# Kernel optimization log

Hardware: AMD Instinct MI355X
Metric: run time of the kernel (lower is better)

## Reference

```python
import jax, jax.numpy as jnp
import numpy as np

HIDDEN = 1024
NUM_HEADS = 16
D_HEAD = HIDDEN // NUM_HEADS  # 64
SEQ = 2048
BATCH = 2


def setup_inputs() -> dict:
    key = jax.random.key(0)
    kx, kw, kb = jax.random.split(key, 3)
    x = jax.random.normal(kx, (SEQ, BATCH, HIDDEN), dtype=jnp.float32)
    W = jax.random.normal(kw, (3 * HIDDEN, HIDDEN), dtype=jnp.float32) * 0.02
    b = jax.random.normal(kb, (3 * HIDDEN,), dtype=jnp.float32) * 0.02
    return {"x": x, "W": W, "b": b}


def reference(x, W, b):
    # x: (S, B, H) seq-first, as in the torch module
    S, B, _ = x.shape
    qkv = jnp.einsum('sbh,oh->sbo', x, W) + b  # (S, B, 3*H)
    # torch views 3*hidden as (num_heads, 3, d_head): per-head-interleaved QKV
    qkv = qkv.reshape(S, B, NUM_HEADS, 3, D_HEAD)
    qkv = jnp.transpose(qkv, (2, 1, 0, 3, 4))  # (nh, B, S, 3, d)
    q, k, v = qkv[..., 0, :], qkv[..., 1, :], qkv[..., 2, :]  # each (nh, B, S, d)
    scale = 1.0 / np.sqrt(D_HEAD).astype(np.float32)
    scores = jnp.einsum('hbqd,hbkd->hbqk', q, k) * scale  # (nh, B, S, S)
    attn = jax.nn.softmax(scores, axis=-1)
    out = jnp.einsum('hbqk,hbkd->hbqd', attn, v)  # (nh, B, S, d)
    out = jnp.transpose(out, (2, 1, 0, 3)).reshape(S, B, HIDDEN)
    return out
```

## Files before the change

### kernel.cpp

```cpp
#include <hip/hip_runtime.h>
#include <hip/hip_bf16.h>


typedef __hip_bfloat16 bf16;
typedef __bf16 bfr;
typedef __attribute__((ext_vector_type(8))) __bf16 bf16x8;
typedef __attribute__((ext_vector_type(4))) __bf16 bf16x4;
typedef __attribute__((ext_vector_type(4))) float f32x4;

#define S_SEQ  2048
#define HID    1024
#define OUT3   3072
#define NROWS  4096
#define LSTR   72

#if __has_builtin(__builtin_amdgcn_exp2f)
#define EXP2F(x) __builtin_amdgcn_exp2f(x)
#else
#define EXP2F(x) exp2f(x)
#endif

#define QSCALE 0.18033688011112042f

__global__ __launch_bounds__(256) void cast_both_kernel(
    const float* __restrict__ X, bfr* __restrict__ Xb,
    const float* __restrict__ W, bfr* __restrict__ Wb)
{
    int bid = blockIdx.x;
    const float* src;
    bfr* dst;
    int lid;
    if (bid < NROWS * HID / 2048) { src = X; dst = Xb; lid = bid; }
    else { src = W; dst = Wb; lid = bid - NROWS * HID / 2048; }
    int gid = lid * 256 + threadIdx.x;
    const float4* s4 = (const float4*)src;
    float4 a = s4[(size_t)gid * 2];
    float4 b = s4[(size_t)gid * 2 + 1];
    bf16x8 v;
    v[0] = (bfr)a.x; v[1] = (bfr)a.y; v[2] = (bfr)a.z; v[3] = (bfr)a.w;
    v[4] = (bfr)b.x; v[5] = (bfr)b.y; v[6] = (bfr)b.z; v[7] = (bfr)b.w;
    *(bf16x8*)(dst + (size_t)gid * 8) = v;
}

__device__ __forceinline__ void gload_lds16(const void* g, void* l) {
    __builtin_amdgcn_global_load_lds(
        (const __attribute__((address_space(1))) unsigned int*)g,
        (__attribute__((address_space(3))) unsigned int*)l, 16, 0, 0);
}

__global__ __launch_bounds__(256, 3) void qkv_gemm_mfma(
    const bfr* __restrict__ Xb, const bfr* __restrict__ Wb,
    const float* __restrict__ bias,
    bfr* __restrict__ qb, bfr* __restrict__ kb, bfr* __restrict__ vtb)
{
    __shared__ __attribute__((aligned(16))) unsigned char lds_all[32768];
    bfr* As = (bfr*)lds_all;
    bfr* Bs = (bfr*)(lds_all + 16384);
    bfr* Tr = (bfr*)lds_all;

    const int o0 = blockIdx.x * 128;
    const int r0 = blockIdx.y * 128;
    const int tid = threadIdx.x;
    const int lane = tid & 63;
    const int w = tid >> 6;
    const int l15 = lane & 15;
    const int quad = lane >> 4;
    const int m0 = (w & 1) * 64;
    const int n0 = (w >> 1) * 64;

    f32x4 acc[4][4];
#pragma unroll
    for (int mi = 0; mi < 4; mi++)
#pragma unroll
        for (int ni = 0; ni < 4; ni++) acc[mi][ni] = {0.f, 0.f, 0.f, 0.f};

    for (int k0 = 0; k0 < HID; k0 += 64) {
#pragma unroll
        for (int i = 0; i < 4; i++) {
            int c = i * 256 + tid;
            int row = c >> 3, c8 = c & 7;
            gload_lds16(Xb + (size_t)(r0 + row) * HID + k0 + c8 * 8, As + c * 8);
            gload_lds16(Wb + (size_t)(o0 + row) * HID + k0 + c8 * 8, Bs + c * 8);
        }
        __syncthreads();

#pragma unroll
        for (int ks = 0; ks < 2; ks++) {
            bf16x8 af[4], bfg[4];
#pragma unroll
            for (int mi = 0; mi < 4; mi++)
                af[mi] = *(const bf16x8*)(As + (m0 + mi * 16 + l15) * 64 + ks * 32 + quad * 8);
#pragma unroll
            for (int ni = 0; ni < 4; ni++)
                bfg[ni] = *(const bf16x8*)(Bs + (n0 + ni * 16 + l15) * 64 + ks * 32 + quad * 8);
#pragma unroll
            for (int mi = 0; mi < 4; mi++)
#pragma unroll
                for (int ni = 0; ni < 4; ni++)
                    acc[mi][ni] = __builtin_amdgcn_mfma_f32_16x16x32_bf16(
                        af[mi], bfg[ni], acc[mi][ni], 0, 0, 0);
        }
        __syncthreads();
    }

    const int omod = o0 % 192;
#pragma unroll
    for (int ni = 0; ni < 4; ni++) {
        int cb = o0 + n0 + ni * 16;
        int h = cb / 192;
        int rem = cb % 192;
        int t = rem >> 6;
        int d = (rem & 63) + l15;
        float bv = bias[cb + l15];
        if (t == 2) {
#pragma unroll
            for (int mi = 0; mi < 4; mi++)
#pragma unroll
                for (int r = 0; r < 4; r++) {
                    int grl = m0 + mi * 16 + quad * 4 + r;
                    Tr[(size_t)d * 144 + (grl & 1) * 72 + (grl >> 1)]
                        = (bfr)(acc[mi][ni][r] + bv);
                }
        } else {
#pragma unroll
            for (int mi = 0; mi < 4; mi++)
#pragma unroll
                for (int r = 0; r < 4; r++) {
                    int gr = r0 + m0 + mi * 16 + quad * 4 + r;
                    int s = gr >> 1, b = gr & 1;
                    int hb = h * 2 + b;
                    float val = acc[mi][ni][r] + bv;
                    if (t == 0)
                        qb[((size_t)hb * S_SEQ + s) * 64 + d] = (bfr)(val * QSCALE);
                    else
                        kb[((size_t)hb * S_SEQ + s) * 64 + d] = (bfr)val;
                }
        }
    }
    if (omod != 0) {
        __syncthreads();
        int ht = (omod == 64) ? (o0 + 64) / 192 : o0 / 192;
        int d = tid >> 2;
        int b = (tid >> 1) & 1;
        int chunk = tid & 1;
        int s0 = r0 >> 1;
        int hb = ht * 2 + b;
        const bfr* src = Tr + (size_t)d * 144 + b * 72 + chunk * 32;
        bfr* dstp = vtb + ((size_t)hb * 64 + d) * S_SEQ + s0 + chunk * 32;
#pragma unroll
        for (int j = 0; j < 4; j++)
            *(bf16x8*)(dstp + j * 8) = *(const bf16x8*)(src + j * 8);
    }
}

__global__ __launch_bounds__(256, 4) void attn4_kernel(
    const bfr* __restrict__ qb, const bfr* __restrict__ kb,
    const bfr* __restrict__ vtb, float* __restrict__ out)
{
    __shared__ __attribute__((aligned(16))) bfr Ks [64 * LSTR];
    __shared__ __attribute__((aligned(16))) bfr Vts[64 * LSTR];
    __shared__ __attribute__((aligned(16))) bfr Ptq[64 * LSTR];

    const int qt = blockIdx.x;
    const int hb = blockIdx.y;
    const int h = hb >> 1, b = hb & 1;
    const int tid = threadIdx.x;
    const int lane = tid & 63;
    const int w = tid >> 6;
    const int l15 = lane & 15;
    const int quad = lane >> 4;
    const size_t hboff = (size_t)hb * S_SEQ * 64;

    const int srow0 = tid >> 3;
    const int sc8   = tid & 7;
    const int qrow = qt * 64 + 16 * w + l15;
    bf16x8 qf[2];
    qf[0] = *(const bf16x8*)(qb + hboff + (size_t)qrow * 64 + quad * 8);
    qf[1] = *(const bf16x8*)(qb + hboff + (size_t)qrow * 64 + quad * 8 + 32);

    f32x4 Oacc[4];
#pragma unroll
    for (int mt = 0; mt < 4; mt++) Oacc[mt] = {0.f, 0.f, 0.f, 0.f};
    float l_st = 0.f;

    bf16x8 kr[2], vr[2];
#pragma unroll
    for (int p = 0; p < 2; p++) {
        int row = srow0 + p * 32;
        kr[p] = *(const bf16x8*)(kb + hboff + (size_t)row * 64 + sc8 * 8);
        vr[p] = *(const bf16x8*)(vtb + hboff + (size_t)row * S_SEQ + sc8 * 8);
    }

    for (int kt = 0; kt < 32; kt++) {
        __syncthreads();
#pragma unroll
        for (int p = 0; p < 2; p++) {
            int row = srow0 + p * 32;
            *(bf16x8*)(Ks  + row * LSTR + sc8 * 8) = kr[p];
            *(bf16x8*)(Vts + row * LSTR + sc8 * 8) = vr[p];
        }
        {
            int ktn = kt + 1 < 32 ? kt + 1 : 31;
#pragma unroll
            for (int p = 0; p < 2; p++) {
                int row = srow0 + p * 32;
                kr[p] = *(const bf16x8*)(kb + hboff + (size_t)(ktn * 64 + row) * 64 + sc8 * 8);
                vr[p] = *(const bf16x8*)(vtb + hboff + (size_t)row * S_SEQ + ktn * 64 + sc8 * 8);
            }
        }
        __syncthreads();

        f32x4 sc[4];
#pragma unroll
        for (int mt = 0; mt < 4; mt++) sc[mt] = {0.f, 0.f, 0.f, 0.f};
#pragma unroll
        for (int k0 = 0; k0 < 2; k0++) {
#pragma unroll
            for (int mt = 0; mt < 4; mt++) {
                bf16x8 kf = *(const bf16x8*)(Ks + (mt * 16 + l15) * LSTR + quad * 8 + 32 * k0);
                sc[mt] = __builtin_amdgcn_mfma_f32_16x16x32_bf16(kf, qf[k0], sc[mt], 0, 0, 0);
            }
        }

        float rs = 0.f;
#pragma unroll
        for (int mt = 0; mt < 4; mt++) {
            bf16x4 pk;
#pragma unroll
            for (int r = 0; r < 4; r++) {
                float pv = EXP2F(sc[mt][r]);
                rs += pv;
                pk[r] = (bfr)pv;
            }
            *(bf16x4*)(Ptq + (16 * w + l15) * LSTR + mt * 16 + quad * 4) = pk;
        }
        rs += __shfl_xor(rs, 16);
        rs += __shfl_xor(rs, 32);
        l_st += rs;

#pragma unroll
        for (int k0 = 0; k0 < 2; k0++) {
            bf16x8 pf = *(const bf16x8*)(Ptq + (16 * w + l15) * LSTR + quad * 8 + 32 * k0);
#pragma unroll
            for (int mt = 0; mt < 4; mt++) {
                bf16x8 vf = *(const bf16x8*)(Vts + (mt * 16 + l15) * LSTR + quad * 8 + 32 * k0);
                Oacc[mt] = __builtin_amdgcn_mfma_f32_16x16x32_bf16(vf, pf, Oacc[mt], 0, 0, 0);
            }
        }
    }

    float inv = 1.0f / l_st;
    float* orow = out + ((size_t)qrow * 2 + b) * HID + h * 64;
#pragma unroll
    for (int mt = 0; mt < 4; mt++) {
        float4 o4;
        o4.x = Oacc[mt][0] * inv;
        o4.y = Oacc[mt][1] * inv;
        o4.z = Oacc[mt][2] * inv;
        o4.w = Oacc[mt][3] * inv;
        *(float4*)(orow + mt * 16 + quad * 4) = o4;
    }
}

extern "C" void kernel_launch(void* const* d_in, const int* in_sizes, int n_in,
                              void* d_out, int out_size, void* d_ws, size_t ws_size,
                              hipStream_t stream) {
    const float* X    = (const float*)d_in[0];
    const float* W    = (const float*)d_in[1];
    const float* bias = (const float*)d_in[2];
    float* out = (float*)d_out;

    bfr* qb  = (bfr*)d_ws;
    bfr* kb  = qb + (size_t)32 * S_SEQ * 64;
    bfr* vtb = kb + (size_t)32 * S_SEQ * 64;

    bfr* Xb = (bfr*)d_out;
    bfr* Wb = Xb + (size_t)NROWS * HID;

    cast_both_kernel<<<(NROWS * HID + OUT3 * HID) / 2048, 256, 0, stream>>>(X, Xb, W, Wb);

    dim3 g1(OUT3 / 128, NROWS / 128);
    qkv_gemm_mfma<<<g1, 256, 0, stream>>>(Xb, Wb, bias, qb, kb, vtb);

    dim3 g2(S_SEQ / 64, 32);
    attn4_kernel<<<g2, 256, 0, stream>>>(qb, kb, vtb, out);
}
```

Baseline: 173.0 us.

## Switch attention to 32x32 MFMA and keep P in registers via permlane swap

Rewrites the attention kernel to use 32x32x16 bf16 MFMA, with each wave handling 32 query rows and each block 128 rows. The softmax probabilities are repacked into B-operand fragments with v_permlane32_swap instead of a round trip through shared memory. This removes the Ptq LDS buffer and its stores and loads, and amortizes each K/V tile over twice as many queries. In exchange it uses more registers (launch bounds lowered to 2 blocks) and launches half as many blocks, which may reduce occupancy and parallelism.

```diff
diff --git a/kernel.cpp b/kernel.cpp
--- a/kernel.cpp
+++ b/kernel.cpp
@@ -6,7 +6,10 @@
 typedef __bf16 bfr;
 typedef __attribute__((ext_vector_type(8))) __bf16 bf16x8;
 typedef __attribute__((ext_vector_type(4))) __bf16 bf16x4;
+typedef __attribute__((ext_vector_type(2))) __bf16 bf16x2;
 typedef __attribute__((ext_vector_type(4))) float f32x4;
+typedef __attribute__((ext_vector_type(16))) float f32x16;
+typedef __attribute__((ext_vector_type(4))) unsigned u32x4;
 
 #define S_SEQ  2048
 #define HID    1024
@@ -153,13 +156,16 @@
     }
 }
 
-__global__ __launch_bounds__(256, 4) void attn4_kernel(
+__device__ __forceinline__ void plswap(unsigned &a, unsigned &b) {
+    asm volatile("v_permlane32_swap_b32 %0, %1" : "+v"(a), "+v"(b));
+}
+
+__global__ __launch_bounds__(256, 2) void attn32_kernel(
     const bfr* __restrict__ qb, const bfr* __restrict__ kb,
     const bfr* __restrict__ vtb, float* __restrict__ out)
 {
     __shared__ __attribute__((aligned(16))) bfr Ks [64 * LSTR];
     __shared__ __attribute__((aligned(16))) bfr Vts[64 * LSTR];
-    __shared__ __attribute__((aligned(16))) bfr Ptq[64 * LSTR];
 
     const int qt = blockIdx.x;
     const int hb = blockIdx.y;
@@ -167,21 +173,25 @@
     const int tid = threadIdx.x;
     const int lane = tid & 63;
     const int w = tid >> 6;
-    const int l15 = lane & 15;
-    const int quad = lane >> 4;
+    const int l31 = lane & 31;
+    const int hi = lane >> 5;
     const size_t hboff = (size_t)hb * S_SEQ * 64;
 
     const int srow0 = tid >> 3;
     const int sc8   = tid & 7;
-    const int qrow = qt * 64 + 16 * w + l15;
-    bf16x8 qf[2];
-    qf[0] = *(const bf16x8*)(qb + hboff + (size_t)qrow * 64 + quad * 8);
-    qf[1] = *(const bf16x8*)(qb + hboff + (size_t)qrow * 64 + quad * 8 + 32);
-
-    f32x4 Oacc[4];
-#pragma unroll
-    for (int mt = 0; mt < 4; mt++) Oacc[mt] = {0.f, 0.f, 0.f, 0.f};
-    float l_st = 0.f;
+
+    const int qrow = qt * 128 + w * 32 + l31;
+    bf16x8 qf[4];
+#pragma unroll
+    for (int kk = 0; kk < 4; kk++)
+        qf[kk] = *(const bf16x8*)(qb + hboff + (size_t)qrow * 64 + kk * 16 + hi * 8);
+
+    f32x16 Oacc[2];
+#pragma unroll
+    for (int dt = 0; dt < 2; dt++)
+#pragma unroll
+        for (int i = 0; i < 16; i++) Oacc[dt][i] = 0.f;
+    float lsum = 0.f;
 
     bf16x8 kr[2], vr[2];
 #pragma unroll
@@ -210,56 +220,66 @@
         }
         __syncthreads();
 
-        f32x4 sc[4];
-#pragma unroll
-        for (int mt = 0; mt < 4; mt++) sc[mt] = {0.f, 0.f, 0.f, 0.f};
-#pragma unroll
-        for (int k0 = 0; k0 < 2; k0++) {
-#pragma unroll
-            for (int mt = 0; mt < 4; mt++) {
-                bf16x8 kf = *(const bf16x8*)(Ks + (mt * 16 + l15) * LSTR + quad * 8 + 32 * k0);
-                sc[mt] = __builtin_amdgcn_mfma_f32_16x16x32_bf16(kf, qf[k0], sc[mt], 0, 0, 0);
+        unsigned wds[2][8];
+        float rs = 0.f;
+#pragma unroll
+        for (int t = 0; t < 2; t++) {
+            f32x16 sc;
+#pragma unroll
+            for (int i = 0; i < 16; i++) sc[i] = 0.f;
+#pragma unroll
+            for (int kk = 0; kk < 4; kk++) {
+                bf16x8 kf = *(const bf16x8*)(Ks + (t * 32 + l31) * LSTR + kk * 16 + hi * 8);
+                sc = __builtin_amdgcn_mfma_f32_32x32x16_bf16(kf, qf[kk], sc, 0, 0, 0);
             }
-        }
-
-        float rs = 0.f;
-#pragma unroll
-        for (int mt = 0; mt < 4; mt++) {
-            bf16x4 pk;
-#pragma unroll
-            for (int r = 0; r < 4; r++) {
-                float pv = EXP2F(sc[mt][r]);
-                rs += pv;
-                pk[r] = (bfr)pv;
+#pragma unroll
+            for (int a = 0; a < 8; a++) {
+                float p0 = EXP2F(sc[2 * a]);
+                float p1 = EXP2F(sc[2 * a + 1]);
+                rs += p0 + p1;
+                bf16x2 pk; pk[0] = (bfr)p0; pk[1] = (bfr)p1;
+                wds[t][a] = __builtin_bit_cast(unsigned, pk);
             }
-            *(bf16x4*)(Ptq + (16 * w + l15) * LSTR + mt * 16 + quad * 4) = pk;
-        }
-        rs += __shfl_xor(rs, 16);
-        rs += __shfl_xor(rs, 32);
-        l_st += rs;
-
-#pragma unroll
-        for (int k0 = 0; k0 < 2; k0++) {
-            bf16x8 pf = *(const bf16x8*)(Ptq + (16 * w + l15) * LSTR + quad * 8 + 32 * k0);
-#pragma unroll
-            for (int mt = 0; mt < 4; mt++) {
-                bf16x8 vf = *(const bf16x8*)(Vts + (mt * 16 + l15) * LSTR + quad * 8 + 32 * k0);
-                Oacc[mt] = __builtin_amdgcn_mfma_f32_16x16x32_bf16(vf, pf, Oacc[mt], 0, 0, 0);
+        }
+        lsum += rs;
+
+        bf16x8 pfrag[4];
+#pragma unroll
+        for (int c = 0; c < 4; c++) {
+            int t = c >> 1, cc = c & 1;
+            unsigned w0 = wds[t][cc * 4 + 0];
+            unsigned w1 = wds[t][cc * 4 + 1];
+            unsigned w2 = wds[t][cc * 4 + 2];
+            unsigned w3 = wds[t][cc * 4 + 3];
+            plswap(w0, w2);
+            plswap(w1, w3);
+            u32x4 pw; pw[0] = w0; pw[1] = w1; pw[2] = w2; pw[3] = w3;
+            pfrag[c] = __builtin_bit_cast(bf16x8, pw);
+        }
+
+#pragma unroll
+        for (int kk = 0; kk < 4; kk++)
+#pragma unroll
+            for (int dt = 0; dt < 2; dt++) {
+                bf16x8 vf = *(const bf16x8*)(Vts + (dt * 32 + l31) * LSTR + kk * 16 + hi * 8);
+                Oacc[dt] = __builtin_amdgcn_mfma_f32_32x32x16_bf16(vf, pfrag[kk], Oacc[dt], 0, 0, 0);
             }
-        }
-    }
-
-    float inv = 1.0f / l_st;
+    }
+
+    lsum += __shfl_xor(lsum, 32);
+    float inv = 1.0f / lsum;
     float* orow = out + ((size_t)qrow * 2 + b) * HID + h * 64;
 #pragma unroll
-    for (int mt = 0; mt < 4; mt++) {
-        float4 o4;
-        o4.x = Oacc[mt][0] * inv;
-        o4.y = Oacc[mt][1] * inv;
-        o4.z = Oacc[mt][2] * inv;
-        o4.w = Oacc[mt][3] * inv;
-        *(float4*)(orow + mt * 16 + quad * 4) = o4;
-    }
+    for (int dt = 0; dt < 2; dt++)
+#pragma unroll
+        for (int g = 0; g < 4; g++) {
+            float4 o4;
+            o4.x = Oacc[dt][4 * g + 0] * inv;
+            o4.y = Oacc[dt][4 * g + 1] * inv;
+            o4.z = Oacc[dt][4 * g + 2] * inv;
+            o4.w = Oacc[dt][4 * g + 3] * inv;
+            *(float4*)(orow + dt * 32 + 8 * g + 4 * hi) = o4;
+        }
 }
 
 extern "C" void kernel_launch(void* const* d_in, const int* in_sizes, int n_in,
@@ -282,6 +302,6 @@
     dim3 g1(OUT3 / 128, NROWS / 128);
     qkv_gemm_mfma<<<g1, 256, 0, stream>>>(Xb, Wb, bias, qb, kb, vtb);
 
-    dim3 g2(S_SEQ / 64, 32);
-    attn4_kernel<<<g2, 256, 0, stream>>>(qb, kb, vtb, out);
-}
+    dim3 g2(S_SEQ / 128, 32);
+    attn32_kernel<<<g2, 256, 0, stream>>>(qb, kb, vtb, out);
+}
```

Measured after the change: 159.5 us. 7.8% less time.
